# Kernel tuning notes

Measured on AMD Instinct MI355X. Metric: run time of the kernel, lower is better.

## Reference

```python
import jax, jax.numpy as jnp
import numpy as np

B, S, D_MODEL, D_HEAD = 4, 4096, 768, 64

def setup_inputs() -> dict:
    key = jax.random.key(0)
    kx, kq, kk, kv = jax.random.split(key, 4)
    scale = 1.0 / np.sqrt(D_MODEL)
    return {
        "x": jax.random.normal(kx, (B, S, D_MODEL), dtype=jnp.float32),
        "W_Q": jax.random.normal(kq, (D_MODEL, D_HEAD), dtype=jnp.float32) * scale,
        "W_K": jax.random.normal(kk, (D_MODEL, D_HEAD), dtype=jnp.float32) * scale,
        "W_V": jax.random.normal(kv, (D_MODEL, D_HEAD), dtype=jnp.float32) * scale,
    }

def reference(x, W_Q, W_K, W_V):
    # x: [B, S, d_model]; projections to [B, S, d_head]
    Q = x @ W_Q
    K = x @ W_K
    V = x @ W_V
    d_head = Q.shape[-1]
    # scores: [B, S, S], scaled dot product
    A = jnp.einsum('bid,bjd->bij', Q, K) / jnp.sqrt(jnp.asarray(d_head, Q.dtype))
    S_len = x.shape[1]
    causal = jnp.tril(jnp.ones((S_len, S_len), dtype=bool))
    A = jnp.where(causal[None, :, :], A, -jnp.inf)
    A = jax.nn.softmax(A, axis=-1)
    return jnp.einsum('bij,bjd->bid', A, V)
```

## Files before the change

### kernel.cpp

```cpp
#include <hip/hip_runtime.h>
#include <hip/hip_bf16.h>

typedef __bf16 bf16_t;
typedef bf16_t bf16x8 __attribute__((ext_vector_type(8)));
typedef float f32x4 __attribute__((ext_vector_type(4)));
typedef float f32x16 __attribute__((ext_vector_type(16)));
typedef unsigned int u32;

#define NB 4
#define SS 4096
#define DM 768
#define DH 64
#define NROW (NB * SS)
#define CSCALE (0.125f * 1.44269504088896341f)
#define MFIX 24.0f

#define QOFF 0u
#define KOFF 2097152u
#define VOFF 4194304u
#define WOFF 6291456u

#define SB() __builtin_amdgcn_sched_barrier(0)

__device__ __forceinline__ u32 cvtpk_bf16(float lo, float hi) {
    u32 r;
    asm volatile("v_cvt_pk_bf16_f32 %0, %1, %2" : "=v"(r) : "v"(lo), "v"(hi));
    return r;
}

__global__ __launch_bounds__(256) void wt_kernel(const float* __restrict__ wq,
                                                 const float* __restrict__ wk,
                                                 const float* __restrict__ wv,
                                                 bf16_t* __restrict__ wt) {
    int id = blockIdx.x * 256 + threadIdx.x;
    if (id >= 3 * DM * DH) return;
    int m = id / (DM * DH);
    int r = id - m * (DM * DH);
    int k = r >> 6;
    int c = r & 63;
    const float* w = (m == 0) ? wq : (m == 1) ? wk : wv;
    wt[(size_t)m * DH * DM + (size_t)c * DM + k] = (bf16_t)w[k * DH + c];
}

__global__ __launch_bounds__(512, 4) void proj_kernel(const float* __restrict__ x,
                                                      const bf16_t* __restrict__ wt,
                                                      bf16_t* __restrict__ Qo,
                                                      bf16_t* __restrict__ Ko,
                                                      bf16_t* __restrict__ Vt) {
    __shared__ __align__(16) float xs[4][2048];

    const int tid = threadIdx.x;
    const int lane = tid & 63;
    const int wid = tid >> 6;
    const int wr = wid & 1;
    const int wc = wid >> 1;
    const int l15 = lane & 15;
    const int g = lane >> 4;
    const int m0 = blockIdx.x * 32;

    const int srow = tid >> 4;
    const int skc = (tid & 15) ^ (srow & 7);
    const float* sbase = x + (size_t)(m0 + srow) * DM + skc * 4;

    #define STAGE(bsel, t_)                                                         \
        __builtin_amdgcn_global_load_lds(                                           \
            (const __attribute__((address_space(1))) void*)(sbase + (t_) * 64),     \
            (__attribute__((address_space(3))) void*)(&xs[bsel][wid * 256]),        \
            16, 0, 0);

    size_t wbase[3];
    #pragma unroll
    for (int n = 0; n < 3; n++) {
        const int gn = wc * 3 + n;
        const int mm = gn >> 2;
        const int cj = gn & 3;
        wbase[n] = (size_t)mm * DH * DM + (size_t)(cj * 16 + l15) * DM + g * 8;
    }

    f32x4 acc[3];
    #pragma unroll
    for (int n = 0; n < 3; n++)
        #pragma unroll
        for (int j = 0; j < 4; j++) acc[n][j] = 0.0f;

    const int arow = wr * 16 + l15;
    int roff[2][2];
    #pragma unroll
    for (int kk = 0; kk < 2; kk++)
        #pragma unroll
        for (int c = 0; c < 2; c++)
            roff[kk][c] = arow * 64 + ((kk * 8 + g * 2 + c) ^ (arow & 7)) * 4;

    bf16x8 wslot[3][3][2];

    #pragma unroll
    for (int n = 0; n < 3; n++)
        #pragma unroll
        for (int kk = 0; kk < 2; kk++)
            wslot[0][n][kk] = *reinterpret_cast<const bf16x8*>(wt + wbase[n] + kk * 32);
    SB();
    STAGE(0, 0); SB();
    #pragma unroll
    for (int n = 0; n < 3; n++)
        #pragma unroll
        for (int kk = 0; kk < 2; kk++)
            wslot[1][n][kk] = *reinterpret_cast<const bf16x8*>(wt + wbase[n] + 64 + kk * 32);
    SB();
    STAGE(1, 1); SB();
    STAGE(2, 2); SB();
    asm volatile("s_waitcnt vmcnt(8)");
    SB();
    __builtin_amdgcn_s_barrier();
    SB();

    #pragma unroll
    for (int t = 0; t < 12; t++) {
        if (t + 2 < 12) {
            #pragma unroll
            for (int n = 0; n < 3; n++)
                #pragma unroll
                for (int kk = 0; kk < 2; kk++)
                    wslot[(t + 2) % 3][n][kk] = *reinterpret_cast<const bf16x8*>(
                        wt + wbase[n] + (t + 2) * 64 + kk * 32);
        }
        SB();
        if (t + 3 < 12) { STAGE((t + 3) & 3, t + 3); }
        SB();
        bf16x8 a[2];
        #pragma unroll
        for (int kk = 0; kk < 2; kk++) {
            f32x4 c0 = *reinterpret_cast<const f32x4*>(&xs[t & 3][roff[kk][0]]);
            f32x4 c1 = *reinterpret_cast<const f32x4*>(&xs[t & 3][roff[kk][1]]);
            bf16x8 tt;
            #pragma unroll
            for (int j = 0; j < 4; j++) { tt[j] = (bf16_t)c0[j]; tt[4 + j] = (bf16_t)c1[j]; }
            a[kk] = tt;
        }
        #pragma unroll
        for (int n = 0; n < 3; n++)
            #pragma unroll
            for (int kk = 0; kk < 2; kk++)
                acc[n] = __builtin_amdgcn_mfma_f32_16x16x32_bf16(a[kk], wslot[t % 3][n][kk], acc[n], 0, 0, 0);

        if (t < 11) {
            if (t <= 8)       { asm volatile("s_waitcnt vmcnt(8)"); }
            else if (t == 9)  { asm volatile("s_waitcnt vmcnt(7)"); }
            else              { asm volatile("s_waitcnt vmcnt(0)"); }
            SB();
            __builtin_amdgcn_s_barrier();
            SB();
        }
    }
    #undef STAGE

    #pragma unroll
    for (int n = 0; n < 3; n++) {
        const int gn = wc * 3 + n;
        const int mm = gn >> 2;
        const int cj = gn & 3;
        #pragma unroll
        for (int j = 0; j < 4; j++) {
            int row = m0 + wr * 16 + g * 4 + j;
            int col = cj * 16 + l15;
            float v = acc[n][j];
            if (mm == 0)      Qo[(size_t)row * DH + col] = (bf16_t)(v * CSCALE);
            else if (mm == 1) Ko[(size_t)row * DH + col] = (bf16_t)v;
            else              Vt[(size_t)col * NROW + row] = (bf16_t)v;
        }
    }
}

__global__ __launch_bounds__(256, 2) void attn_kernel(const bf16_t* __restrict__ Q,
                                                      const bf16_t* __restrict__ K,
                                                      const bf16_t* __restrict__ Vt,
                                                      float* __restrict__ out) {
    __shared__ float Ob[2][2][16][64];
    __shared__ float Ls[2][64];

    const int tid = threadIdx.x;
    const int lane = tid & 63;
    const int w = tid >> 6;
    const int l31 = lane & 31;
    const int hi = lane >> 5;
    const int bx = blockIdx.x;
    const int b = (bx & 7) >> 1;
    const int r_ = (bx >> 3) * 2 + (bx & 1);
    const int tile = (r_ < 64) ? (127 - r_) : (r_ - 64);
    const int q0 = tile * 32;
    const int nkv = (tile >> 1) + 1;
    const int q = q0 + l31;

    const bf16_t* Qb = Q + (size_t)b * SS * DH;
    const bf16_t* Kb = K + (size_t)b * SS * DH;
    const bf16_t* Vb = Vt + (size_t)b * SS;

    bf16x8 bq[4];
    #pragma unroll
    for (int ks = 0; ks < 4; ks++)
        bq[ks] = *reinterpret_cast<const bf16x8*>(
            Qb + (size_t)(q0 + l31) * DH + ks * 16 + hi * 8);

    f32x16 o[2];
    #pragma unroll
    for (int c = 0; c < 2; c++)
        #pragma unroll
        for (int r = 0; r < 16; r++) o[c][r] = 0.0f;
    float lsum = 0.0f;

    for (int kt = w; kt < nkv; kt += 4) {
        const int kv0 = kt * 64;
        const bool diag = (kv0 + 63 > q0);

        bf16x8 ak0[4];
        #pragma unroll
        for (int ks = 0; ks < 4; ks++)
            ak0[ks] = *reinterpret_cast<const bf16x8*>(
                Kb + (size_t)(kv0 + l31) * DH + ks * 16 + hi * 8);
        SB();
        bf16x8 ak1[4];
        #pragma unroll
        for (int ks = 0; ks < 4; ks++)
            ak1[ks] = *reinterpret_cast<const bf16x8*>(
                Kb + (size_t)(kv0 + 32 + l31) * DH + ks * 16 + hi * 8);
        SB();
        bf16x8 vf[2][4];
        #pragma unroll
        for (int c = 0; c < 2; c++)
            #pragma unroll
            for (int kks = 0; kks < 4; kks++)
                vf[c][kks] = *reinterpret_cast<const bf16x8*>(
                    Vb + (size_t)(c * 32 + l31) * NROW + kv0 + kks * 16 + hi * 8);
        SB();

        u32 pa[4][4];
        f32x16 s0;
        #pragma unroll
        for (int r = 0; r < 16; r++) s0[r] = 0.0f;
        #pragma unroll
        for (int ks = 0; ks < 4; ks++)
            s0 = __builtin_amdgcn_mfma_f32_32x32x16_bf16(ak0[ks], bq[ks], s0, 0, 0, 0);
        f32x16 s1;
        #pragma unroll
        for (int r = 0; r < 16; r++) s1[r] = 0.0f;
        #pragma unroll
        for (int ks = 0; ks < 4; ks++)
            s1 = __builtin_amdgcn_mfma_f32_32x32x16_bf16(ak1[ks], bq[ks], s1, 0, 0, 0);

        #pragma unroll
        for (int blk = 0; blk < 2; blk++) {
            const f32x16& s = blk ? s1 : s0;
            const int kvbase = kv0 + blk * 32 + 4 * hi;
            float p[16];
            #pragma unroll
            for (int r = 0; r < 16; r++) {
                float e = exp2f(s[r] - MFIX);
                if (diag) {
                    int kv = kvbase + (r & 3) + 8 * (r >> 2);
                    e = (kv > q) ? 0.0f : e;
                }
                p[r] = e;
                lsum += e;
            }
            #pragma unroll
            for (int ks2 = 0; ks2 < 2; ks2++) {
                u32 w01 = cvtpk_bf16(p[8 * ks2 + 0], p[8 * ks2 + 1]);
                u32 w23 = cvtpk_bf16(p[8 * ks2 + 2], p[8 * ks2 + 3]);
                u32 w45 = cvtpk_bf16(p[8 * ks2 + 4], p[8 * ks2 + 5]);
                u32 w67 = cvtpk_bf16(p[8 * ks2 + 6], p[8 * ks2 + 7]);
                asm volatile("v_permlane32_swap_b32 %0, %1" : "+v"(w01), "+v"(w45));
                asm volatile("v_permlane32_swap_b32 %0, %1" : "+v"(w23), "+v"(w67));
                pa[blk * 2 + ks2][0] = w01;
                pa[blk * 2 + ks2][1] = w23;
                pa[blk * 2 + ks2][2] = w45;
                pa[blk * 2 + ks2][3] = w67;
            }
        }

        #pragma unroll
        for (int kks = 0; kks < 4; kks++) {
            union { u32 w4[4]; bf16x8 v; } uu;
            uu.w4[0] = pa[kks][0];
            uu.w4[1] = pa[kks][1];
            uu.w4[2] = pa[kks][2];
            uu.w4[3] = pa[kks][3];
            #pragma unroll
            for (int c = 0; c < 2; c++)
                o[c] = __builtin_amdgcn_mfma_f32_32x32x16_bf16(uu.v, vf[c][kks], o[c], 0, 0, 0);
        }
    }

    if (w >= 2) {
        #pragma unroll
        for (int c = 0; c < 2; c++)
            #pragma unroll
            for (int r = 0; r < 16; r++) Ob[w - 2][c][r][lane] = o[c][r];
        Ls[w - 2][lane] = lsum;
    }
    __syncthreads();
    if (w < 2) {
        #pragma unroll
        for (int c = 0; c < 2; c++)
            #pragma unroll
            for (int r = 0; r < 16; r++) o[c][r] += Ob[w][c][r][lane];
        lsum += Ls[w][lane];
    }
    __syncthreads();
    if (w == 1) {
        #pragma unroll
        for (int c = 0; c < 2; c++)
            #pragma unroll
            for (int r = 0; r < 16; r++) Ob[0][c][r][lane] = o[c][r];
        Ls[0][lane] = lsum;
    }
    __syncthreads();
    if (w == 0) {
        #pragma unroll
        for (int c = 0; c < 2; c++)
            #pragma unroll
            for (int r = 0; r < 16; r++) o[c][r] += Ob[0][c][r][lane];
        lsum += Ls[0][lane];

        float lfull = lsum + __shfl_xor(lsum, 32);
        float* ob = out + ((size_t)b * SS + q0) * DH;
        #pragma unroll
        for (int c = 0; c < 2; c++)
            #pragma unroll
            for (int r = 0; r < 16; r++) {
                const int qr = (r & 3) + 8 * (r >> 2) + 4 * hi;
                float lr = __shfl(lfull, qr);
                ob[(size_t)qr * DH + c * 32 + l31] = o[c][r] / lr;
            }
    }
}

extern "C" void kernel_launch(void* const* d_in, const int* in_sizes, int n_in,
                              void* d_out, int out_size, void* d_ws, size_t ws_size,
                              hipStream_t stream) {
    const float* x  = (const float*)d_in[0];
    const float* wq = (const float*)d_in[1];
    const float* wk = (const float*)d_in[2];
    const float* wv = (const float*)d_in[3];
    float* out = (float*)d_out;

    char* ws = (char*)d_ws;
    bf16_t* Qw = (bf16_t*)(ws + QOFF);
    bf16_t* Kw = (bf16_t*)(ws + KOFF);
    bf16_t* Vt = (bf16_t*)(ws + VOFF);
    bf16_t* Wt = (bf16_t*)(ws + WOFF);

    hipLaunchKernelGGL(wt_kernel, dim3((3 * DM * DH + 255) / 256), dim3(256), 0, stream,
                       wq, wk, wv, Wt);
    hipLaunchKernelGGL(proj_kernel, dim3(NROW / 32), dim3(512), 0, stream,
                       x, Wt, Qw, Kw, Vt);
    hipLaunchKernelGGL(attn_kernel, dim3(NB * 128), dim3(256), 0, stream,
                       Qw, Kw, Vt, out);
}
```

Measured before the change: 81.68 us.

## Load projection x tiles straight to registers instead of LDS staging

The projection kernel stops staging x through shared memory with global_load_lds and per-iteration barriers. Each lane now loads its own fp32 x fragments directly into a 4-deep register ring alongside the weight ring, which removes LDS traffic and block-wide s_barrier syncs. Occupancy bounds are lowered to fit the larger register footprint. The cost is redundant x loads across the wave columns that share rows, plus higher register pressure.

```diff
diff --git a/kernel.cpp b/kernel.cpp
--- a/kernel.cpp
+++ b/kernel.cpp
@@ -42,13 +42,11 @@
     wt[(size_t)m * DH * DM + (size_t)c * DM + k] = (bf16_t)w[k * DH + c];
 }
 
-__global__ __launch_bounds__(512, 4) void proj_kernel(const float* __restrict__ x,
+__global__ __launch_bounds__(512, 2) void proj_kernel(const float* __restrict__ x,
                                                       const bf16_t* __restrict__ wt,
                                                       bf16_t* __restrict__ Qo,
                                                       bf16_t* __restrict__ Ko,
                                                       bf16_t* __restrict__ Vt) {
-    __shared__ __align__(16) float xs[4][2048];
-
     const int tid = threadIdx.x;
     const int lane = tid & 63;
     const int wid = tid >> 6;
@@ -58,15 +56,7 @@
     const int g = lane >> 4;
     const int m0 = blockIdx.x * 32;
 
-    const int srow = tid >> 4;
-    const int skc = (tid & 15) ^ (srow & 7);
-    const float* sbase = x + (size_t)(m0 + srow) * DM + skc * 4;
-
-    #define STAGE(bsel, t_)                                                         \
-        __builtin_amdgcn_global_load_lds(                                           \
-            (const __attribute__((address_space(1))) void*)(sbase + (t_) * 64),     \
-            (__attribute__((address_space(3))) void*)(&xs[bsel][wid * 256]),        \
-            16, 0, 0);
+    const float* xb = x + (size_t)(m0 + wr * 16 + l15) * DM + g * 8;
 
     size_t wbase[3];
     #pragma unroll
@@ -83,75 +73,59 @@
         #pragma unroll
         for (int j = 0; j < 4; j++) acc[n][j] = 0.0f;
 
-    const int arow = wr * 16 + l15;
-    int roff[2][2];
-    #pragma unroll
-    for (int kk = 0; kk < 2; kk++)
-        #pragma unroll
-        for (int c = 0; c < 2; c++)
-            roff[kk][c] = arow * 64 + ((kk * 8 + g * 2 + c) ^ (arow & 7)) * 4;
-
-    bf16x8 wslot[3][3][2];
-
-    #pragma unroll
-    for (int n = 0; n < 3; n++)
-        #pragma unroll
-        for (int kk = 0; kk < 2; kk++)
-            wslot[0][n][kk] = *reinterpret_cast<const bf16x8*>(wt + wbase[n] + kk * 32);
-    SB();
-    STAGE(0, 0); SB();
-    #pragma unroll
-    for (int n = 0; n < 3; n++)
-        #pragma unroll
-        for (int kk = 0; kk < 2; kk++)
-            wslot[1][n][kk] = *reinterpret_cast<const bf16x8*>(wt + wbase[n] + 64 + kk * 32);
-    SB();
-    STAGE(1, 1); SB();
-    STAGE(2, 2); SB();
-    asm volatile("s_waitcnt vmcnt(8)");
-    SB();
-    __builtin_amdgcn_s_barrier();
-    SB();
+    f32x4 xsl[4][2][2];
+    bf16x8 wsl[3][3][2];
+
+    #define ISSUE_W(slot, t_)                                                       \
+        {                                                                           \
+            _Pragma("unroll")                                                       \
+            for (int n = 0; n < 3; n++)                                             \
+                _Pragma("unroll")                                                   \
+                for (int kk = 0; kk < 2; kk++)                                      \
+                    wsl[slot][n][kk] = *reinterpret_cast<const bf16x8*>(            \
+                        wt + wbase[n] + (t_) * 64 + kk * 32);                       \
+        }
+    #define ISSUE_X(slot, t_)                                                       \
+        {                                                                           \
+            _Pragma("unroll")                                                       \
+            for (int kk = 0; kk < 2; kk++)                                          \
+                _Pragma("unroll")                                                   \
+                for (int h = 0; h < 2; h++)                                         \
+                    xsl[slot][kk][h] = *reinterpret_cast<const f32x4*>(             \
+                        xb + (t_) * 64 + kk * 32 + h * 4);                          \
+        }
+
+    ISSUE_W(0, 0); SB();
+    ISSUE_W(1, 1); SB();
+    ISSUE_X(0, 0); SB();
+    ISSUE_X(1, 1); SB();
+    ISSUE_X(2, 2); SB();
 
     #pragma unroll
     for (int t = 0; t < 12; t++) {
-        if (t + 2 < 12) {
-            #pragma unroll
-            for (int n = 0; n < 3; n++)
-                #pragma unroll
-                for (int kk = 0; kk < 2; kk++)
-                    wslot[(t + 2) % 3][n][kk] = *reinterpret_cast<const bf16x8*>(
-                        wt + wbase[n] + (t + 2) * 64 + kk * 32);
-        }
-        SB();
-        if (t + 3 < 12) { STAGE((t + 3) & 3, t + 3); }
+        if (t + 2 < 12) { ISSUE_W((t + 2) % 3, t + 2); }
+        SB();
+        if (t + 3 < 12) { ISSUE_X((t + 3) & 3, t + 3); }
         SB();
         bf16x8 a[2];
         #pragma unroll
         for (int kk = 0; kk < 2; kk++) {
-            f32x4 c0 = *reinterpret_cast<const f32x4*>(&xs[t & 3][roff[kk][0]]);
-            f32x4 c1 = *reinterpret_cast<const f32x4*>(&xs[t & 3][roff[kk][1]]);
             bf16x8 tt;
             #pragma unroll
-            for (int j = 0; j < 4; j++) { tt[j] = (bf16_t)c0[j]; tt[4 + j] = (bf16_t)c1[j]; }
+            for (int j = 0; j < 4; j++) {
+                tt[j] = (bf16_t)xsl[t & 3][kk][0][j];
+                tt[4 + j] = (bf16_t)xsl[t & 3][kk][1][j];
+            }
             a[kk] = tt;
         }
         #pragma unroll
         for (int n = 0; n < 3; n++)
             #pragma unroll
             for (int kk = 0; kk < 2; kk++)
-                acc[n] = __builtin_amdgcn_mfma_f32_16x16x32_bf16(a[kk], wslot[t % 3][n][kk], acc[n], 0, 0, 0);
-
-        if (t < 11) {
-            if (t <= 8)       { asm volatile("s_waitcnt vmcnt(8)"); }
-            else if (t == 9)  { asm volatile("s_waitcnt vmcnt(7)"); }
-            else              { asm volatile("s_waitcnt vmcnt(0)"); }
-            SB();
-            __builtin_amdgcn_s_barrier();
-            SB();
-        }
-    }
-    #undef STAGE
+                acc[n] = __builtin_amdgcn_mfma_f32_16x16x32_bf16(a[kk], wsl[t % 3][n][kk], acc[n], 0, 0, 0);
+    }
+    #undef ISSUE_W
+    #undef ISSUE_X
 
     #pragma unroll
     for (int n = 0; n < 3; n++) {
```

Measured after the change: 99.84 us. 1.22x slower.

## Split attention KV range across two blocks and deepen projection staging pipeline

Applied to the files above, without the earlier changes.

Each query tile's causal KV loop is split across two workgroups (8 waves total), which doubles the grid from 512 to 1024 blocks to improve CU occupancy and balance. The two halves combine through global partial buffers and an atomic flag, so the second block to finish sums both partials and normalizes. The projection kernel also stages x tiles five deep instead of three, using 8 LDS buffers with adjusted vmcnt waits and lower launch-bound occupancy. The split adds a memset, extra global traffic for partials and fences, and only runs if the workspace is large enough.

```diff
diff --git a/kernel.cpp b/kernel.cpp
--- a/kernel.cpp
+++ b/kernel.cpp
@@ -19,6 +19,10 @@
 #define KOFF 2097152u
 #define VOFF 4194304u
 #define WOFF 6291456u
+#define FOFF 6586368u
+#define POFF 6590464u
+#define PART_F32 2112
+#define WS_NEED (POFF + 1024ull * 8448ull)
 
 #define SB() __builtin_amdgcn_sched_barrier(0)
 
@@ -42,12 +46,12 @@
     wt[(size_t)m * DH * DM + (size_t)c * DM + k] = (bf16_t)w[k * DH + c];
 }
 
-__global__ __launch_bounds__(512, 4) void proj_kernel(const float* __restrict__ x,
+__global__ __launch_bounds__(512, 2) void proj_kernel(const float* __restrict__ x,
                                                       const bf16_t* __restrict__ wt,
                                                       bf16_t* __restrict__ Qo,
                                                       bf16_t* __restrict__ Ko,
                                                       bf16_t* __restrict__ Vt) {
-    __shared__ __align__(16) float xs[4][2048];
+    __shared__ __align__(16) float xs[8][2048];
 
     const int tid = threadIdx.x;
     const int lane = tid & 63;
@@ -108,7 +112,9 @@
     SB();
     STAGE(1, 1); SB();
     STAGE(2, 2); SB();
-    asm volatile("s_waitcnt vmcnt(8)");
+    STAGE(3, 3); SB();
+    STAGE(4, 4); SB();
+    asm volatile("s_waitcnt vmcnt(10)");
     SB();
     __builtin_amdgcn_s_barrier();
     SB();
@@ -124,13 +130,13 @@
                         wt + wbase[n] + (t + 2) * 64 + kk * 32);
         }
         SB();
-        if (t + 3 < 12) { STAGE((t + 3) & 3, t + 3); }
+        if (t + 5 < 12) { STAGE((t + 5) & 7, t + 5); }
         SB();
         bf16x8 a[2];
         #pragma unroll
         for (int kk = 0; kk < 2; kk++) {
-            f32x4 c0 = *reinterpret_cast<const f32x4*>(&xs[t & 3][roff[kk][0]]);
-            f32x4 c1 = *reinterpret_cast<const f32x4*>(&xs[t & 3][roff[kk][1]]);
+            f32x4 c0 = *reinterpret_cast<const f32x4*>(&xs[t & 7][roff[kk][0]]);
+            f32x4 c1 = *reinterpret_cast<const f32x4*>(&xs[t & 7][roff[kk][1]]);
             bf16x8 tt;
             #pragma unroll
             for (int j = 0; j < 4; j++) { tt[j] = (bf16_t)c0[j]; tt[4 + j] = (bf16_t)c1[j]; }
@@ -143,9 +149,11 @@
                 acc[n] = __builtin_amdgcn_mfma_f32_16x16x32_bf16(a[kk], wslot[t % 3][n][kk], acc[n], 0, 0, 0);
 
         if (t < 11) {
-            if (t <= 8)       { asm volatile("s_waitcnt vmcnt(8)"); }
-            else if (t == 9)  { asm volatile("s_waitcnt vmcnt(7)"); }
-            else              { asm volatile("s_waitcnt vmcnt(0)"); }
+            if (t <= 6)       { asm volatile("s_waitcnt vmcnt(10)"); }
+            else if (t == 7)  { asm volatile("s_waitcnt vmcnt(9)");  }
+            else if (t == 8)  { asm volatile("s_waitcnt vmcnt(8)");  }
+            else if (t == 9)  { asm volatile("s_waitcnt vmcnt(7)");  }
+            else              { asm volatile("s_waitcnt vmcnt(0)");  }
             SB();
             __builtin_amdgcn_s_barrier();
             SB();
@@ -170,10 +178,13 @@
     }
 }
 
-__global__ __launch_bounds__(256, 2) void attn_kernel(const bf16_t* __restrict__ Q,
-                                                      const bf16_t* __restrict__ K,
-                                                      const bf16_t* __restrict__ Vt,
-                                                      float* __restrict__ out) {
+template<bool SPLIT>
+__global__ __launch_bounds__(256) void attn_kernel(const bf16_t* __restrict__ Q,
+                                                   const bf16_t* __restrict__ K,
+                                                   const bf16_t* __restrict__ Vt,
+                                                   float* __restrict__ out,
+                                                   float* __restrict__ part,
+                                                   int* __restrict__ flags) {
     __shared__ float Ob[2][2][16][64];
     __shared__ float Ls[2][64];
 
@@ -183,8 +194,10 @@
     const int l31 = lane & 31;
     const int hi = lane >> 5;
     const int bx = blockIdx.x;
-    const int b = (bx & 7) >> 1;
-    const int r_ = (bx >> 3) * 2 + (bx & 1);
+
+    int b, h, r_;
+    if (SPLIT) { b = bx & 3; int rest = bx >> 2; h = rest & 1; r_ = rest >> 1; }
+    else       { b = (bx & 7) >> 1; h = 0; r_ = (bx >> 3) * 2 + (bx & 1); }
     const int tile = (r_ < 64) ? (127 - r_) : (r_ - 64);
     const int q0 = tile * 32;
     const int nkv = (tile >> 1) + 1;
@@ -207,7 +220,10 @@
         for (int r = 0; r < 16; r++) o[c][r] = 0.0f;
     float lsum = 0.0f;
 
-    for (int kt = w; kt < nkv; kt += 4) {
+    const int c0 = SPLIT ? (h * 4 + w) : w;
+    const int cstride = SPLIT ? 8 : 4;
+
+    for (int kt = c0; kt < nkv; kt += cstride) {
         const int kv0 = kt * 64;
         const bool diag = (kv0 + 63 > q0);
 
@@ -313,24 +329,47 @@
         Ls[0][lane] = lsum;
     }
     __syncthreads();
-    if (w == 0) {
-        #pragma unroll
-        for (int c = 0; c < 2; c++)
-            #pragma unroll
-            for (int r = 0; r < 16; r++) o[c][r] += Ob[0][c][r][lane];
-        lsum += Ls[0][lane];
-
-        float lfull = lsum + __shfl_xor(lsum, 32);
-        float* ob = out + ((size_t)b * SS + q0) * DH;
-        #pragma unroll
-        for (int c = 0; c < 2; c++)
-            #pragma unroll
-            for (int r = 0; r < 16; r++) {
-                const int qr = (r & 3) + 8 * (r >> 2) + 4 * hi;
-                float lr = __shfl(lfull, qr);
-                ob[(size_t)qr * DH + c * 32 + l31] = o[c][r] / lr;
-            }
-    }
+    if (w != 0) return;
+
+    #pragma unroll
+    for (int c = 0; c < 2; c++)
+        #pragma unroll
+        for (int r = 0; r < 16; r++) o[c][r] += Ob[0][c][r][lane];
+    lsum += Ls[0][lane];
+
+    if (SPLIT) {
+        const int fid = b * 128 + tile;
+        const int pid = fid * 2 + h;
+        float* P = part + (size_t)pid * PART_F32;
+        #pragma unroll
+        for (int c = 0; c < 2; c++)
+            #pragma unroll
+            for (int r = 0; r < 16; r++) P[(c * 16 + r) * 64 + lane] = o[c][r];
+        P[2048 + lane] = lsum;
+        __threadfence();
+        int old = 0;
+        if (lane == 0) old = atomicAdd(&flags[fid], 1);
+        old = __shfl(old, 0);
+        if (old == 0) return;
+        __threadfence();
+        const float* Po = part + (size_t)(pid ^ 1) * PART_F32;
+        #pragma unroll
+        for (int c = 0; c < 2; c++)
+            #pragma unroll
+            for (int r = 0; r < 16; r++) o[c][r] += Po[(c * 16 + r) * 64 + lane];
+        lsum += Po[2048 + lane];
+    }
+
+    float lfull = lsum + __shfl_xor(lsum, 32);
+    float* ob = out + ((size_t)b * SS + q0) * DH;
+    #pragma unroll
+    for (int c = 0; c < 2; c++)
+        #pragma unroll
+        for (int r = 0; r < 16; r++) {
+            const int qr = (r & 3) + 8 * (r >> 2) + 4 * hi;
+            float lr = __shfl(lfull, qr);
+            ob[(size_t)qr * DH + c * 32 + l31] = o[c][r] / lr;
+        }
 }
 
 extern "C" void kernel_launch(void* const* d_in, const int* in_sizes, int n_in,
@@ -347,11 +386,20 @@
     bf16_t* Kw = (bf16_t*)(ws + KOFF);
     bf16_t* Vt = (bf16_t*)(ws + VOFF);
     bf16_t* Wt = (bf16_t*)(ws + WOFF);
+    int*    flags = (int*)(ws + FOFF);
+    float*  part  = (float*)(ws + POFF);
 
     hipLaunchKernelGGL(wt_kernel, dim3((3 * DM * DH + 255) / 256), dim3(256), 0, stream,
                        wq, wk, wv, Wt);
     hipLaunchKernelGGL(proj_kernel, dim3(NROW / 32), dim3(512), 0, stream,
                        x, Wt, Qw, Kw, Vt);
-    hipLaunchKernelGGL(attn_kernel, dim3(NB * 128), dim3(256), 0, stream,
-                       Qw, Kw, Vt, out);
+
+    if (ws_size >= WS_NEED) {
+        hipMemsetAsync(flags, 0, 512 * sizeof(int), stream);
+        hipLaunchKernelGGL((attn_kernel<true>), dim3(NB * 128 * 2), dim3(256), 0, stream,
+                           Qw, Kw, Vt, out, part, flags);
+    } else {
+        hipLaunchKernelGGL((attn_kernel<false>), dim3(NB * 128), dim3(256), 0, stream,
+                           Qw, Kw, Vt, out, part, flags);
+    }
 }
```

Result: slower. 139.8 us (+71.2%).

## Double-buffer K/V register loads to prefetch next tile during compute

Applied to the files above, without the earlier changes.

Splits the KV loop body into ISSUE (global loads of K and V fragments into registers) and CONSUME (QK MFMA, exp/mask, PV MFMA) macros. Two register buffer sets A and B alternate, so the loads for tile kt+4 are issued before tile kt is computed. This hides global-load latency behind MFMA work, but roughly doubles the VGPRs held for K/V fragments, which may lower occupancy or cause spills.

```diff
diff --git a/kernel.cpp b/kernel.cpp
--- a/kernel.cpp
+++ b/kernel.cpp
@@ -207,87 +207,105 @@
         for (int r = 0; r < 16; r++) o[c][r] = 0.0f;
     float lsum = 0.0f;
 
-    for (int kt = w; kt < nkv; kt += 4) {
-        const int kv0 = kt * 64;
-        const bool diag = (kv0 + 63 > q0);
-
-        bf16x8 ak0[4];
-        #pragma unroll
-        for (int ks = 0; ks < 4; ks++)
-            ak0[ks] = *reinterpret_cast<const bf16x8*>(
-                Kb + (size_t)(kv0 + l31) * DH + ks * 16 + hi * 8);
-        SB();
-        bf16x8 ak1[4];
-        #pragma unroll
-        for (int ks = 0; ks < 4; ks++)
-            ak1[ks] = *reinterpret_cast<const bf16x8*>(
-                Kb + (size_t)(kv0 + 32 + l31) * DH + ks * 16 + hi * 8);
-        SB();
-        bf16x8 vf[2][4];
-        #pragma unroll
-        for (int c = 0; c < 2; c++)
-            #pragma unroll
-            for (int kks = 0; kks < 4; kks++)
-                vf[c][kks] = *reinterpret_cast<const bf16x8*>(
-                    Vb + (size_t)(c * 32 + l31) * NROW + kv0 + kks * 16 + hi * 8);
-        SB();
-
-        u32 pa[4][4];
-        f32x16 s0;
-        #pragma unroll
-        for (int r = 0; r < 16; r++) s0[r] = 0.0f;
-        #pragma unroll
-        for (int ks = 0; ks < 4; ks++)
-            s0 = __builtin_amdgcn_mfma_f32_32x32x16_bf16(ak0[ks], bq[ks], s0, 0, 0, 0);
-        f32x16 s1;
-        #pragma unroll
-        for (int r = 0; r < 16; r++) s1[r] = 0.0f;
-        #pragma unroll
-        for (int ks = 0; ks < 4; ks++)
-            s1 = __builtin_amdgcn_mfma_f32_32x32x16_bf16(ak1[ks], bq[ks], s1, 0, 0, 0);
-
-        #pragma unroll
-        for (int blk = 0; blk < 2; blk++) {
-            const f32x16& s = blk ? s1 : s0;
-            const int kvbase = kv0 + blk * 32 + 4 * hi;
-            float p[16];
-            #pragma unroll
-            for (int r = 0; r < 16; r++) {
-                float e = exp2f(s[r] - MFIX);
-                if (diag) {
-                    int kv = kvbase + (r & 3) + 8 * (r >> 2);
-                    e = (kv > q) ? 0.0f : e;
-                }
-                p[r] = e;
-                lsum += e;
-            }
-            #pragma unroll
-            for (int ks2 = 0; ks2 < 2; ks2++) {
-                u32 w01 = cvtpk_bf16(p[8 * ks2 + 0], p[8 * ks2 + 1]);
-                u32 w23 = cvtpk_bf16(p[8 * ks2 + 2], p[8 * ks2 + 3]);
-                u32 w45 = cvtpk_bf16(p[8 * ks2 + 4], p[8 * ks2 + 5]);
-                u32 w67 = cvtpk_bf16(p[8 * ks2 + 6], p[8 * ks2 + 7]);
-                asm volatile("v_permlane32_swap_b32 %0, %1" : "+v"(w01), "+v"(w45));
-                asm volatile("v_permlane32_swap_b32 %0, %1" : "+v"(w23), "+v"(w67));
-                pa[blk * 2 + ks2][0] = w01;
-                pa[blk * 2 + ks2][1] = w23;
-                pa[blk * 2 + ks2][2] = w45;
-                pa[blk * 2 + ks2][3] = w67;
-            }
-        }
-
-        #pragma unroll
-        for (int kks = 0; kks < 4; kks++) {
-            union { u32 w4[4]; bf16x8 v; } uu;
-            uu.w4[0] = pa[kks][0];
-            uu.w4[1] = pa[kks][1];
-            uu.w4[2] = pa[kks][2];
-            uu.w4[3] = pa[kks][3];
-            #pragma unroll
-            for (int c = 0; c < 2; c++)
-                o[c] = __builtin_amdgcn_mfma_f32_32x32x16_bf16(uu.v, vf[c][kks], o[c], 0, 0, 0);
-        }
-    }
+    bf16x8 akA0[4], akA1[4], vfA[2][4];
+    bf16x8 akB0[4], akB1[4], vfB[2][4];
+
+    #define ISSUE(S, kt_) do {                                                      \
+        const int kvI = (kt_) * 64;                                                 \
+        _Pragma("unroll")                                                           \
+        for (int ks = 0; ks < 4; ks++)                                              \
+            ak##S##0[ks] = *reinterpret_cast<const bf16x8*>(                        \
+                Kb + (size_t)(kvI + l31) * DH + ks * 16 + hi * 8);                  \
+        SB();                                                                       \
+        _Pragma("unroll")                                                           \
+        for (int ks = 0; ks < 4; ks++)                                              \
+            ak##S##1[ks] = *reinterpret_cast<const bf16x8*>(                        \
+                Kb + (size_t)(kvI + 32 + l31) * DH + ks * 16 + hi * 8);             \
+        SB();                                                                       \
+        _Pragma("unroll")                                                           \
+        for (int c = 0; c < 2; c++)                                                 \
+            _Pragma("unroll")                                                       \
+            for (int kks = 0; kks < 4; kks++)                                       \
+                vf##S[c][kks] = *reinterpret_cast<const bf16x8*>(                   \
+                    Vb + (size_t)(c * 32 + l31) * NROW + kvI + kks * 16 + hi * 8);  \
+        SB();                                                                       \
+    } while (0)
+
+    #define CONSUME(S, kt_) do {                                                    \
+        const int kv0 = (kt_) * 64;                                                 \
+        const bool diag = (kv0 + 63 > q0);                                          \
+        u32 pa[4][4];                                                               \
+        f32x16 s0;                                                                  \
+        _Pragma("unroll")                                                           \
+        for (int r = 0; r < 16; r++) s0[r] = 0.0f;                                  \
+        _Pragma("unroll")                                                           \
+        for (int ks = 0; ks < 4; ks++)                                              \
+            s0 = __builtin_amdgcn_mfma_f32_32x32x16_bf16(ak##S##0[ks], bq[ks], s0, 0, 0, 0); \
+        f32x16 s1;                                                                  \
+        _Pragma("unroll")                                                           \
+        for (int r = 0; r < 16; r++) s1[r] = 0.0f;                                  \
+        _Pragma("unroll")                                                           \
+        for (int ks = 0; ks < 4; ks++)                                              \
+            s1 = __builtin_amdgcn_mfma_f32_32x32x16_bf16(ak##S##1[ks], bq[ks], s1, 0, 0, 0); \
+        _Pragma("unroll")                                                           \
+        for (int blk = 0; blk < 2; blk++) {                                         \
+            const f32x16& s = blk ? s1 : s0;                                        \
+            const int kvbase = kv0 + blk * 32 + 4 * hi;                             \
+            float p[16];                                                            \
+            _Pragma("unroll")                                                       \
+            for (int r = 0; r < 16; r++) {                                          \
+                float e = exp2f(s[r] - MFIX);                                       \
+                if (diag) {                                                         \
+                    int kv = kvbase + (r & 3) + 8 * (r >> 2);                       \
+                    e = (kv > q) ? 0.0f : e;                                        \
+                }                                                                   \
+                p[r] = e;                                                           \
+                lsum += e;                                                          \
+            }                                                                       \
+            _Pragma("unroll")                                                       \
+            for (int ks2 = 0; ks2 < 2; ks2++) {                                     \
+                u32 w01 = cvtpk_bf16(p[8 * ks2 + 0], p[8 * ks2 + 1]);               \
+                u32 w23 = cvtpk_bf16(p[8 * ks2 + 2], p[8 * ks2 + 3]);               \
+                u32 w45 = cvtpk_bf16(p[8 * ks2 + 4], p[8 * ks2 + 5]);               \
+                u32 w67 = cvtpk_bf16(p[8 * ks2 + 6], p[8 * ks2 + 7]);               \
+                asm volatile("v_permlane32_swap_b32 %0, %1" : "+v"(w01), "+v"(w45)); \
+                asm volatile("v_permlane32_swap_b32 %0, %1" : "+v"(w23), "+v"(w67)); \
+                pa[blk * 2 + ks2][0] = w01;                                         \
+                pa[blk * 2 + ks2][1] = w23;                                         \
+                pa[blk * 2 + ks2][2] = w45;                                         \
+                pa[blk * 2 + ks2][3] = w67;                                         \
+            }                                                                       \
+        }                                                                           \
+        _Pragma("unroll")                                                           \
+        for (int kks = 0; kks < 4; kks++) {                                         \
+            union { u32 w4[4]; bf16x8 v; } uu;                                      \
+            uu.w4[0] = pa[kks][0];                                                  \
+            uu.w4[1] = pa[kks][1];                                                  \
+            uu.w4[2] = pa[kks][2];                                                  \
+            uu.w4[3] = pa[kks][3];                                                  \
+            _Pragma("unroll")                                                       \
+            for (int c = 0; c < 2; c++)                                             \
+                o[c] = __builtin_amdgcn_mfma_f32_32x32x16_bf16(uu.v, vf##S[c][kks], o[c], 0, 0, 0); \
+        }                                                                           \
+    } while (0)
+
+    int kt = w;
+    if (kt < nkv) {
+        ISSUE(A, kt);
+        for (;;) {
+            int ktB = kt + 4;
+            if (ktB < nkv) ISSUE(B, ktB);
+            CONSUME(A, kt);
+            if (ktB >= nkv) break;
+            int ktA = ktB + 4;
+            if (ktA < nkv) ISSUE(A, ktA);
+            CONSUME(B, ktB);
+            if (ktA >= nkv) break;
+            kt = ktA;
+        }
+    }
+    #undef ISSUE
+    #undef CONSUME
 
     if (w >= 2) {
         #pragma unroll
```

After: 87.26 us. +6.8%, slower.
